# Kernel optimization log

Measured on AMD Instinct MI355X. Metric: run time of the kernel, lower is better.

## Reference

```python
import jax, jax.numpy as jnp
import numpy as np

IN_C, OUT_C, K, STRIDE, PAD = 64, 128, 3, 1, 1


def setup_inputs() -> dict:
    key = jax.random.key(0)
    kx, kw = jax.random.split(key)
    x = jax.random.normal(kx, (16, IN_C, 112, 112), dtype=jnp.float32)
    scale = np.sqrt(2.0 / (IN_C * K * K)).astype(np.float32)
    weight = jax.random.normal(kw, (OUT_C, IN_C, K, K), dtype=jnp.float32) * scale
    bias = jnp.zeros((OUT_C,), dtype=jnp.float32)
    return {"x": x, "weight": weight, "bias": bias}


def reference(x, weight, bias):
    # Direct 2D convolution (cross-correlation, like torch Conv2d), NCHW layout.
    out = jax.lax.conv_general_dilated(
        x, weight,
        window_strides=(STRIDE, STRIDE),
        padding=((PAD, PAD), (PAD, PAD)),
        dimension_numbers=("NCHW", "OIHW", "NCHW"),
    )
    return out + bias[None, :, None, None]
```

## Files before the change

### kernel.cpp

```cpp
#include <hip/hip_runtime.h>
#include <stdint.h>


#define HW     112
#define PIX    12544
#define ICN    64
#define OCN    128
#define TILEP  128
#define PTILES 98
#define NBLK   1568
#define NIMG   16

#define XT_BYTES   (NIMG * PIX * ICN * 2)
#define WT_OFF     XT_BYTES
#define WT_BYTES   (9 * OCN * ICN * 2)
#define ZG_OFF     (WT_OFF + WT_BYTES)
#define XBLK       (NIMG * (PIX / 64))
#define WBLK       72

typedef __attribute__((ext_vector_type(8))) __bf16 bf16x8;
typedef __attribute__((ext_vector_type(4))) float  f32x4;

__device__ __forceinline__ uint32_t rne_lo(float f) {
    uint32_t u = __builtin_bit_cast(uint32_t, f);
    return (u + 0x7fffu + ((u >> 16) & 1u)) >> 16;
}
__device__ __forceinline__ uint32_t pk2(float a, float b) {
    uint32_t ub = __builtin_bit_cast(uint32_t, b);
    ub = (ub + 0x7fffu + ((ub >> 16) & 1u)) & 0xffff0000u;
    return rne_lo(a) | ub;
}

__device__ __forceinline__ void load_lds16(const void* g, void* l) {
    __builtin_amdgcn_global_load_lds(
        (const __attribute__((address_space(1))) uint32_t*)g,
        (__attribute__((address_space(3))) uint32_t*)l, 16, 0, 0);
}

__global__ void __launch_bounds__(256)
prep(const float* __restrict__ x, const float* __restrict__ w, uint8_t* __restrict__ ws) {
    const int b = blockIdx.x;
    const int t = threadIdx.x;
    uint16_t* xt = (uint16_t*)ws;
    uint16_t* wt = (uint16_t*)(ws + WT_OFF);

    if (b < XBLK) {
        const int n  = b / (PIX / 64);
        const int p0 = (b - n * (PIX / 64)) * 64;
        const int px = t >> 2;
        const int q  = t & 3;
        const float* src = x + ((size_t)n * ICN + q * 16) * PIX + p0 + px;
        float v[16];
#pragma unroll
        for (int i = 0; i < 16; ++i) v[i] = src[(size_t)i * PIX];
        uint4 u0 = make_uint4(pk2(v[0], v[1]),  pk2(v[2], v[3]),
                              pk2(v[4], v[5]),  pk2(v[6], v[7]));
        uint4 u1 = make_uint4(pk2(v[8], v[9]),  pk2(v[10], v[11]),
                              pk2(v[12], v[13]), pk2(v[14], v[15]));
        char* dst = (char*)xt + ((size_t)(n * PIX + p0 + px)) * 128 + q * 32;
        *(uint4*)dst        = u0;
        *(uint4*)(dst + 16) = u1;
    } else {
        const int wb = b - XBLK;
#pragma unroll
        for (int k = 0; k < 4; ++k) {
            int wi = wb * 1024 + k * 256 + t;
            int r  = wi >> 13;
            int oc = (wi >> 6) & 127;
            int ic = wi & 63;
            wt[wi] = (uint16_t)rne_lo(w[oc * 576 + ic * 9 + r]);
        }
        if (wb == 0 && t < 8) ((uint4*)(ws + ZG_OFF))[t] = make_uint4(0, 0, 0, 0);
    }
}

__global__ void __launch_bounds__(256)
conv_mfma(const uint8_t* __restrict__ ws, const float* __restrict__ bias,
          float* __restrict__ out) {
    __shared__ uint16_t As[2][8192];
    __shared__ uint16_t Xs[2][8192];

    const char* xt = (const char*)ws;
    const char* wt = (const char*)(ws + WT_OFF);
    const char* zg = (const char*)(ws + ZG_OFF);

    const int t = threadIdx.x;
    const int b = (blockIdx.x & 7) * (NBLK / 8) + (blockIdx.x >> 3);
    const int n_img = b / PTILES;
    const int p0 = (b - n_img * PTILES) * TILEP;

    const int lane = t & 63;
    const int wave = t >> 6;
    const int lr = lane & 15;
    const int lq = lane >> 4;
    const int oc_base = (wave & 1) * 64;
    const int px_base = (wave >> 1) * 64;

    const int rowB = t >> 3;
    const int cswz = (t & 7) ^ (rowB & 7);
    int sh[4], sw[4];
    const char* xaddr[4];
#pragma unroll
    for (int r2 = 0; r2 < 4; ++r2) {
        int row = r2 * 32 + rowB;
        int p = p0 + row;
        int hh = p / HW;
        sh[r2] = hh;
        sw[r2] = p - hh * HW;
        xaddr[r2] = xt + ((size_t)(n_img * PIX + p)) * 128 + cswz * 16;
    }
    const char* waddr0 = wt + rowB * 128 + cswz * 16;
    const char* zaddr  = zg + (t & 7) * 16;

    auto stage = [&](int tap, int bsel) {
        const int dy = tap / 3 - 1;
        const int dx = tap - (tap / 3) * 3 - 1;
        const int toff = (dy * HW + dx) * 128;
#pragma unroll
        for (int r2 = 0; r2 < 4; ++r2)
            load_lds16(waddr0 + tap * 16384 + r2 * 4096,
                       (char*)As[bsel] + r2 * 4096 + wave * 1024);
#pragma unroll
        for (int r2 = 0; r2 < 4; ++r2) {
            int hh = sh[r2] + dy;
            int wwp = sw[r2] + dx;
            bool ok = ((unsigned)hh < HW) & ((unsigned)wwp < HW);
            const char* gp = ok ? (xaddr[r2] + toff) : zaddr;
            load_lds16(gp, (char*)Xs[bsel] + r2 * 4096 + wave * 1024);
        }
    };

    f32x4 acc[4][4];
    {
        f32x4 z = {0.f, 0.f, 0.f, 0.f};
#pragma unroll
        for (int i = 0; i < 4; ++i)
#pragma unroll
            for (int j = 0; j < 4; ++j) acc[i][j] = z;
    }

    stage(0, 0);

#pragma unroll
    for (int tap = 0; tap < 9; ++tap) {
        __builtin_amdgcn_sched_barrier(0);
        __builtin_amdgcn_s_barrier();

        if (tap < 8) stage(tap + 1, (tap + 1) & 1);
        __builtin_amdgcn_sched_barrier(0);
        if (tap < 8) asm volatile("s_waitcnt vmcnt(8)" ::: "memory");
        else         asm volatile("s_waitcnt vmcnt(0)" ::: "memory");
        __builtin_amdgcn_sched_barrier(0);

        __builtin_amdgcn_s_barrier();

        const char* Ab = (const char*)As[tap & 1];
        const char* Xb = (const char*)Xs[tap & 1];
#pragma unroll
        for (int kh = 0; kh < 2; ++kh) {
            bf16x8 a_frag[4], b_frag[4];
            const int cc = kh * 4 + lq;
#pragma unroll
            for (int mi = 0; mi < 4; ++mi) {
                int R = oc_base + mi * 16 + lr;
                a_frag[mi] = *(const bf16x8*)(Ab + R * 128 + ((cc ^ (R & 7)) * 16));
            }
#pragma unroll
            for (int ni = 0; ni < 4; ++ni) {
                int R = px_base + ni * 16 + lr;
                b_frag[ni] = *(const bf16x8*)(Xb + R * 128 + ((cc ^ (R & 7)) * 16));
            }
#pragma unroll
            for (int mi = 0; mi < 4; ++mi)
#pragma unroll
                for (int ni = 0; ni < 4; ++ni)
                    acc[mi][ni] = __builtin_amdgcn_mfma_f32_16x16x32_bf16(
                        a_frag[mi], b_frag[ni], acc[mi][ni], 0, 0, 0);
        }
    }

#pragma unroll
    for (int mi = 0; mi < 4; ++mi) {
#pragma unroll
        for (int rg = 0; rg < 4; ++rg) {
            const int oc = oc_base + mi * 16 + lq * 4 + rg;
            const float bb = bias[oc];
            float* orow = out + ((size_t)n_img * OCN + oc) * PIX + p0 + px_base + lr;
#pragma unroll
            for (int ni = 0; ni < 4; ++ni)
                orow[ni * 16] = acc[mi][ni][rg] + bb;
        }
    }
}

extern "C" void kernel_launch(void* const* d_in, const int* in_sizes, int n_in,
                              void* d_out, int out_size, void* d_ws, size_t ws_size,
                              hipStream_t stream) {
    const float* x    = (const float*)d_in[0];
    const float* w    = (const float*)d_in[1];
    const float* bias = (const float*)d_in[2];
    float* out = (float*)d_out;
    uint8_t* ws = (uint8_t*)d_ws;

    prep<<<XBLK + WBLK, 256, 0, stream>>>(x, w, ws);
    conv_mfma<<<NBLK, 256, 0, stream>>>(ws, bias, out);
}
```

Measured before the change: 170.0 us.

## Reuse a haloed input window across dx taps instead of reloading per tap

Instead of loading a fresh 128-pixel input tile for each of the nine taps, the kernel loads a 160-row window once per kernel row (dy) and reuses it for the three dx shifts. It indexes into that window with per-lane row offsets and falls back to a zero row for out-of-bounds pixels. This cuts global-to-LDS input traffic roughly threefold, and the wait counts are retuned to match. It also wraps the MFMA block in s_setprio, and the correctness of the swizzle with shifted rows and the vmcnt accounting are delicate.

```diff
diff --git a/kernel.cpp b/kernel.cpp
--- a/kernel.cpp
+++ b/kernel.cpp
@@ -17,6 +17,9 @@
 #define ZG_OFF     (WT_OFF + WT_BYTES)
 #define XBLK       (NIMG * (PIX / 64))
 #define WBLK       72
+
+#define XW_ZROW    160
+#define XW_BYTES   (161 * 128)
 
 typedef __attribute__((ext_vector_type(8))) __bf16 bf16x8;
 typedef __attribute__((ext_vector_type(4))) float  f32x4;
@@ -78,7 +81,7 @@
 conv_mfma(const uint8_t* __restrict__ ws, const float* __restrict__ bias,
           float* __restrict__ out) {
     __shared__ uint16_t As[2][8192];
-    __shared__ uint16_t Xs[2][8192];
+    __shared__ __align__(16) uint8_t Xw[2][XW_BYTES];
 
     const char* xt = (const char*)ws;
     const char* wt = (const char*)(ws + WT_OFF);
@@ -98,37 +101,39 @@
 
     const int rowB = t >> 3;
     const int cswz = (t & 7) ^ (rowB & 7);
-    int sh[4], sw[4];
-    const char* xaddr[4];
-#pragma unroll
-    for (int r2 = 0; r2 < 4; ++r2) {
-        int row = r2 * 32 + rowB;
-        int p = p0 + row;
-        int hh = p / HW;
-        sh[r2] = hh;
-        sw[r2] = p - hh * HW;
-        xaddr[r2] = xt + ((size_t)(n_img * PIX + p)) * 128 + cswz * 16;
-    }
+    const char* xsrcX  = xt + ((size_t)n_img * PIX) * 128 + cswz * 16;
     const char* waddr0 = wt + rowB * 128 + cswz * 16;
     const char* zaddr  = zg + (t & 7) * 16;
 
-    auto stage = [&](int tap, int bsel) {
-        const int dy = tap / 3 - 1;
-        const int dx = tap - (tap / 3) * 3 - 1;
-        const int toff = (dy * HW + dx) * 128;
+    int hh[4], wwp[4], rbase[4];
+#pragma unroll
+    for (int ni = 0; ni < 4; ++ni) {
+        int po = px_base + ni * 16 + lr;
+        int p  = p0 + po;
+        int h  = p / HW;
+        hh[ni]   = h;
+        wwp[ni]  = p - h * HW;
+        rbase[ni] = po + 1;
+    }
+
+    auto stageW = [&](int tap, int bsel) {
 #pragma unroll
         for (int r2 = 0; r2 < 4; ++r2)
             load_lds16(waddr0 + tap * 16384 + r2 * 4096,
                        (char*)As[bsel] + r2 * 4096 + wave * 1024);
-#pragma unroll
-        for (int r2 = 0; r2 < 4; ++r2) {
-            int hh = sh[r2] + dy;
-            int wwp = sw[r2] + dx;
-            bool ok = ((unsigned)hh < HW) & ((unsigned)wwp < HW);
-            const char* gp = ok ? (xaddr[r2] + toff) : zaddr;
-            load_lds16(gp, (char*)Xs[bsel] + r2 * 4096 + wave * 1024);
-        }
     };
+    auto stageX = [&](int g, int bsel) {
+        const int pwb = p0 + (g - 1) * HW - 1;
+#pragma unroll
+        for (int r2 = 0; r2 < 5; ++r2) {
+            int pw = pwb + r2 * 32 + rowB;
+            const char* gp = ((unsigned)pw < PIX) ? (xsrcX + (ptrdiff_t)pw * 128) : zaddr;
+            load_lds16(gp, (char*)Xw[bsel] + r2 * 4096 + wave * 1024);
+        }
+    };
+
+    if (t < 16)
+        *(uint4*)((char*)Xw[t >> 3] + XW_ZROW * 128 + (t & 7) * 16) = make_uint4(0, 0, 0, 0);
 
     f32x4 acc[4][4];
     {
@@ -139,43 +144,62 @@
             for (int j = 0; j < 4; ++j) acc[i][j] = z;
     }
 
-    stage(0, 0);
+    stageX(0, 0);
+    stageW(0, 0);
+    __syncthreads();
 
 #pragma unroll
     for (int tap = 0; tap < 9; ++tap) {
+        const int g  = tap / 3;
+        const int dy = g - 1;
+        const int dx = tap - g * 3 - 1;
+
         __builtin_amdgcn_sched_barrier(0);
         __builtin_amdgcn_s_barrier();
 
-        if (tap < 8) stage(tap + 1, (tap + 1) & 1);
+        if (tap < 8) stageW(tap + 1, (tap + 1) & 1);
+        if (tap == 0) stageX(1, 1);
+        if (tap == 3) stageX(2, 0);
         __builtin_amdgcn_sched_barrier(0);
-        if (tap < 8) asm volatile("s_waitcnt vmcnt(8)" ::: "memory");
-        else         asm volatile("s_waitcnt vmcnt(0)" ::: "memory");
+        if (tap == 0 || tap == 1 || tap == 3 || tap == 4)
+            asm volatile("s_waitcnt vmcnt(9)" ::: "memory");
+        else if (tap == 8)
+            asm volatile("s_waitcnt vmcnt(0)" ::: "memory");
+        else
+            asm volatile("s_waitcnt vmcnt(4)" ::: "memory");
         __builtin_amdgcn_sched_barrier(0);
 
         __builtin_amdgcn_s_barrier();
 
+        int ro[4];
+#pragma unroll
+        for (int ni = 0; ni < 4; ++ni) {
+            bool ok = ((unsigned)(hh[ni] + dy) < HW) & ((unsigned)(wwp[ni] + dx) < HW);
+            ro[ni] = ok ? (rbase[ni] + dx) : XW_ZROW;
+        }
+
         const char* Ab = (const char*)As[tap & 1];
-        const char* Xb = (const char*)Xs[tap & 1];
+        const char* Xb = (const char*)Xw[g & 1];
 #pragma unroll
         for (int kh = 0; kh < 2; ++kh) {
+            const int cc = kh * 4 + lq;
             bf16x8 a_frag[4], b_frag[4];
-            const int cc = kh * 4 + lq;
 #pragma unroll
             for (int mi = 0; mi < 4; ++mi) {
                 int R = oc_base + mi * 16 + lr;
                 a_frag[mi] = *(const bf16x8*)(Ab + R * 128 + ((cc ^ (R & 7)) * 16));
             }
 #pragma unroll
-            for (int ni = 0; ni < 4; ++ni) {
-                int R = px_base + ni * 16 + lr;
-                b_frag[ni] = *(const bf16x8*)(Xb + R * 128 + ((cc ^ (R & 7)) * 16));
-            }
+            for (int ni = 0; ni < 4; ++ni)
+                b_frag[ni] = *(const bf16x8*)(Xb + ro[ni] * 128 + ((cc ^ (ro[ni] & 7)) * 16));
+            __builtin_amdgcn_s_setprio(1);
 #pragma unroll
             for (int mi = 0; mi < 4; ++mi)
 #pragma unroll
                 for (int ni = 0; ni < 4; ++ni)
                     acc[mi][ni] = __builtin_amdgcn_mfma_f32_16x16x32_bf16(
                         a_frag[mi], b_frag[ni], acc[mi][ni], 0, 0, 0);
+            __builtin_amdgcn_s_setprio(0);
         }
     }
 
```

Measured after the change: 172.1 us. About the same (+1.3%).
